# Optimization experiments

Measured on AMD Instinct MI355X. Metric: run time of the kernel, lower is better.

The kernel has to match this reference:

```python
import jax, jax.numpy as jnp
import numpy as np

B, DIM, H = 65536, 1024, 16
HD = DIM // H  # head dim = 64


def setup_inputs() -> dict:
    key = jax.random.key(0)
    ks = jax.random.split(key, 6)
    x = jax.random.normal(ks[0], (B, DIM), dtype=jnp.float32)
    y = jax.random.normal(ks[1], (B, DIM), dtype=jnp.float32)
    mask = jnp.zeros((B,), dtype=jnp.bool_)  # unused by the module
    # Parameters (qkv_bias=False -> no bias on q/kv; proj has bias)
    Wq = jax.random.normal(ks[2], (DIM, DIM), dtype=jnp.float32) * 0.02
    Wkv = jax.random.normal(ks[3], (DIM, 2 * DIM), dtype=jnp.float32) * 0.02
    Wproj = jax.random.normal(ks[4], (DIM, DIM), dtype=jnp.float32) * 0.02
    bproj = jax.random.normal(ks[5], (DIM,), dtype=jnp.float32) * 0.02
    return {"x": x, "y": y, "mask": mask, "Wq": Wq, "Wkv": Wkv,
            "Wproj": Wproj, "bproj": bproj}


def reference(x, y, mask, Wq, Wkv, Wproj, bproj):
    # mask is accepted but unused, matching the original module.
    scale = HD ** (-0.5)
    q = x @ Wq                      # [B, DIM]
    kv = y @ Wkv                    # [B, 2*DIM]
    k, v = jnp.split(kv, 2, axis=-1)
    # b (h d) -> b h d
    q = q.reshape(B, H, HD) * scale  # first scale (q *= scale)
    k = k.reshape(B, H, HD)
    v = v.reshape(B, H, HD)
    # per-head dot product, scaled AGAIN (faithful to original double-scale)
    dots = jnp.einsum("bhd,bhd->bh", q, k) * scale  # [B, H]
    attn = jax.nn.softmax(dots, axis=-1)             # softmax over heads
    out = attn[..., None] * v                        # [B, H, HD]
    out = out.reshape(B, DIM)                        # b h d -> b (h d)
    return out @ Wproj + bproj
```

## Files before the change

kernel.cpp:

```cpp
#include <hip/hip_runtime.h>

typedef unsigned short ushort_t;
typedef unsigned int   uint_t;

typedef ushort_t u16x8  __attribute__((ext_vector_type(8)));
typedef __bf16   bf16x8 __attribute__((ext_vector_type(8)));
typedef float    f32x4  __attribute__((ext_vector_type(4)));

#define DIMSZ 1024

__device__ __forceinline__ ushort_t f2bf(float f) {
  uint_t u = __builtin_bit_cast(uint_t, f);
  u += 0x7fffu + ((u >> 16) & 1u);
  return (ushort_t)(u >> 16);
}
__device__ __forceinline__ float bf2f(ushort_t h) {
  uint_t u = ((uint_t)h) << 16;
  return __builtin_bit_cast(float, u);
}
__device__ __forceinline__ void lds_load16(const void* g, void* l) {
  __builtin_amdgcn_global_load_lds((const __attribute__((address_space(1))) void*)g,
                                   (__attribute__((address_space(3))) void*)l, 16, 0, 0);
}
#define SCHED0() __builtin_amdgcn_sched_barrier(0)
#define WBAR() do { SCHED0(); __builtin_amdgcn_s_barrier(); SCHED0(); } while (0)

__global__ __launch_bounds__(256) void wtrans(const float* __restrict__ src, int ld,
                                              ushort_t* __restrict__ dst) {
  __shared__ ushort_t tile[32][33];
  const int bx = blockIdx.x, by = blockIdx.y;
  const int tx = threadIdx.x & 31, ty = threadIdx.x >> 5;
#pragma unroll
  for (int i = 0; i < 32; i += 8)
    tile[ty + i][tx] = f2bf(src[(size_t)(by * 32 + ty + i) * ld + bx * 32 + tx]);
  __syncthreads();
#pragma unroll
  for (int i = 0; i < 32; i += 8)
    dst[(size_t)(bx * 32 + ty + i) * 1024 + by * 32 + tx] = tile[tx][ty + i];
}

__global__ __launch_bounds__(256) void cvt_bf16(const float* __restrict__ s,
                                                ushort_t* __restrict__ d) {
  const size_t n8 = (size_t)65536 * 1024 / 8;
  const size_t stride = (size_t)gridDim.x * 256;
  for (size_t i = (size_t)blockIdx.x * 256 + threadIdx.x; i < n8; i += stride) {
    f32x4 f0 = *(const f32x4*)(s + i * 8);
    f32x4 f1 = *(const f32x4*)(s + i * 8 + 4);
    u16x8 o;
#pragma unroll
    for (int j = 0; j < 4; ++j) { o[j] = f2bf(f0[j]); o[4 + j] = f2bf(f1[j]); }
    *(u16x8*)(d + i * 8) = o;
  }
}

__global__ __launch_bounds__(256) void softmax16(float* __restrict__ d) {
  const int row = blockIdx.x * 256 + threadIdx.x;
  f32x4 v[4];
#pragma unroll
  for (int i = 0; i < 4; ++i) v[i] = *(const f32x4*)(d + (size_t)row * 16 + i * 4);
  float m = v[0][0];
#pragma unroll
  for (int i = 0; i < 4; ++i)
#pragma unroll
    for (int j = 0; j < 4; ++j) m = fmaxf(m, v[i][j]);
  float sum = 0.f;
#pragma unroll
  for (int i = 0; i < 4; ++i)
#pragma unroll
    for (int j = 0; j < 4; ++j) { v[i][j] = expf(v[i][j] - m); sum += v[i][j]; }
  const float r = 1.f / sum;
#pragma unroll
  for (int i = 0; i < 4; ++i) {
#pragma unroll
    for (int j = 0; j < 4; ++j) v[i][j] *= r;
    *(f32x4*)(d + (size_t)row * 16 + i * 4) = v[i];
  }
}

__global__ __launch_bounds__(256) void abk(const ushort_t* __restrict__ kvb,
                                           const float* __restrict__ at,
                                           ushort_t* __restrict__ ab) {
  const size_t stride = (size_t)gridDim.x * 256;
  for (size_t g = (size_t)blockIdx.x * 256 + threadIdx.x; g < (size_t)8388608; g += stride) {
    const int row = (int)(g >> 7), c8 = (int)(g & 127);
    const float sc = at[(size_t)row * 16 + (c8 >> 3)];
    u16x8 v8 = *(const u16x8*)(kvb + (size_t)row * 2048 + 1024 + c8 * 8);
    u16x8 o;
#pragma unroll
    for (int j = 0; j < 8; ++j) o[j] = f2bf(bf2f(v8[j]) * sc);
    *(u16x8*)(ab + (size_t)row * 1024 + c8 * 8) = o;
  }
}

template <int EPI>
__global__ __launch_bounds__(512, 2) void gemm8(const ushort_t* __restrict__ A,
                                                const ushort_t* __restrict__ Bt,
                                                void* __restrict__ Cv,
                                                const float* __restrict__ bias,
                                                const ushort_t* __restrict__ kvp,
                                                float* __restrict__ dots,
                                                int ldc, int ncol_lg2) {
  __shared__ ushort_t lds[65536];
  const int t = threadIdx.x;
  const int nb8 = gridDim.x >> 3;
  const int nbid = (blockIdx.x & 7) * nb8 + (blockIdx.x >> 3);
  const int n0 = (nbid & ((1 << ncol_lg2) - 1)) * 256;
  const int m0 = (nbid >> ncol_lg2) * 256;
  const int w = t >> 6, lane = t & 63;
  const int wm = w >> 2, wn = w & 3;
  const int lr = lane & 15, lk = lane >> 4;

  const int sr = lane >> 3;
  const int scsw = ((lane & 7) * 16) ^ ((sr & 7) << 4);
  const ushort_t* aS = A + (size_t)(m0 + w * 8 + sr) * DIMSZ + (scsw >> 1);
  const ushort_t* bS = Bt + (size_t)(n0 + w * 8 + sr) * DIMSZ + (scsw >> 1);

  const int cbe0 = ((lk * 16) ^ ((lr & 7) << 4)) >> 1;
  const int cbe1 = ((64 + lk * 16) ^ ((lr & 7) << 4)) >> 1;
  const int aRowB = (wm * 128 + lr) * 64;
  const int bRowB = 16384 + (wn * 64 + lr) * 64;

  f32x4 acc[8][4];
  const f32x4 zf = {0.f, 0.f, 0.f, 0.f};
#pragma unroll
  for (int i = 0; i < 8; ++i)
#pragma unroll
    for (int j = 0; j < 4; ++j) acc[i][j] = zf;
  bf16x8 a[4][2], b[4][2];

#define STG(cc, tt) do {                                                    \
    _Pragma("unroll") for (int i_ = 0; i_ < 4; ++i_)                        \
      lds_load16(aS + (size_t)i_ * 64 * DIMSZ + (tt) * 64,                  \
                 lds + (cc) * 32768 + (i_ * 64 + w * 8) * 64);              \
    _Pragma("unroll") for (int i_ = 0; i_ < 4; ++i_)                        \
      lds_load16(bS + (size_t)i_ * 64 * DIMSZ + (tt) * 64,                  \
                 lds + (cc) * 32768 + 16384 + (i_ * 64 + w * 8) * 64);      \
  } while (0)
#define LDA4(cc, mq) do {                                                   \
    const ushort_t* Lp = lds + (cc) * 32768 + aRowB + (mq) * 4096;          \
    _Pragma("unroll") for (int j = 0; j < 4; ++j) {                         \
      a[j][0] = *(const bf16x8*)(Lp + j * 1024 + cbe0);                     \
      a[j][1] = *(const bf16x8*)(Lp + j * 1024 + cbe1); } } while (0)
#define LDB4(cc) do {                                                       \
    const ushort_t* Lp = lds + (cc) * 32768 + bRowB;                        \
    _Pragma("unroll") for (int ni = 0; ni < 4; ++ni) {                      \
      b[ni][0] = *(const bf16x8*)(Lp + ni * 1024 + cbe0);                   \
      b[ni][1] = *(const bf16x8*)(Lp + ni * 1024 + cbe1); } } while (0)
#define MMQ(mb) do {                                                        \
    _Pragma("unroll") for (int j = 0; j < 4; ++j)                           \
    _Pragma("unroll") for (int ni = 0; ni < 4; ++ni)                        \
    _Pragma("unroll") for (int ks = 0; ks < 2; ++ks)                        \
      acc[(mb) + j][ni] = __builtin_amdgcn_mfma_f32_16x16x32_bf16(          \
          a[j][ks], b[ni][ks], acc[(mb) + j][ni], 0, 0, 0); } while (0)
#define TILE(S, VM, tv, cc) do {                                            \
    LDB4(cc);                                                               \
    LDA4(cc, 0);                                                            \
    __builtin_amdgcn_s_setprio(1); MMQ(0); __builtin_amdgcn_s_setprio(0);   \
    LDA4(cc, 1);                                                            \
    __builtin_amdgcn_s_setprio(1); MMQ(4); __builtin_amdgcn_s_setprio(0);   \
    WBAR();                                                                 \
    if (S) STG(cc, (tv) + 2);                                               \
    if ((VM) == 8)      asm volatile("s_waitcnt vmcnt(8)" ::: "memory");    \
    else if ((VM) == 0) asm volatile("s_waitcnt vmcnt(0)" ::: "memory");    \
    WBAR();                                                                 \
  } while (0)

  STG(0, 0); STG(1, 1);
  asm volatile("s_waitcnt vmcnt(8)" ::: "memory");
  WBAR();

  for (int tt = 0; tt < 7; ++tt) {
    const int t0 = tt * 2;
    TILE(1, 8, t0, 0);
    TILE(1, 8, t0 + 1, 1);
  }
  TILE(0, 0, 14, 0);
  TILE(0, -1, 15, 1);

#undef TILE
#undef MMQ
#undef LDB4
#undef LDA4
#undef STG

  if constexpr (EPI == 0) {
    ushort_t* Cp = (ushort_t*)Cv;
    ushort_t* ep = lds + w * 8192;
#pragma unroll
    for (int mq = 0; mq < 2; ++mq)
#pragma unroll
      for (int j = 0; j < 4; ++j)
#pragma unroll
        for (int ni = 0; ni < 4; ++ni)
#pragma unroll
          for (int r = 0; r < 4; ++r) {
            const int row = mq * 64 + j * 16 + lk * 4 + r;
            const int ce = ((ni * 16 + lr) * 2) ^ ((row & 7) << 4);
            ep[row * 64 + (ce >> 1)] = f2bf(acc[mq * 4 + j][ni][r]);
          }
#pragma unroll
    for (int rr = 0; rr < 16; ++rr) {
      const int row = rr * 8 + (lane >> 3);
      const int ce = ((lane & 7) * 16) ^ ((lane >> 3) << 4);
      u16x8 vv = *(const u16x8*)(ep + row * 64 + (ce >> 1));
      *(u16x8*)(Cp + (size_t)(m0 + wm * 128 + row) * ldc + n0 + wn * 64 + (lane & 7) * 8) = vv;
    }
  } else if constexpr (EPI == 1) {
    float* Op = (float*)Cv;
    float bb[4];
#pragma unroll
    for (int ni = 0; ni < 4; ++ni) bb[ni] = bias[n0 + wn * 64 + ni * 16 + lr];
#pragma unroll
    for (int mq = 0; mq < 2; ++mq)
#pragma unroll
      for (int j = 0; j < 4; ++j)
#pragma unroll
        for (int ni = 0; ni < 4; ++ni)
#pragma unroll
          for (int r = 0; r < 4; ++r)
            Op[(size_t)(m0 + wm * 128 + mq * 64 + j * 16 + lk * 4 + r) * 1024 +
               n0 + wn * 64 + ni * 16 + lr] = acc[mq * 4 + j][ni][r] + bb[ni];
  } else {
    const int h = (n0 >> 6) + wn;
    ushort_t* kw = lds + w * 8192;
    const int rsub = lane >> 3, c8 = (lane & 7) * 8;
    const ushort_t* kS = kvp + (size_t)(m0 + wm * 128 + rsub) * 2048 + h * 64 + c8;
#pragma unroll
    for (int i = 0; i < 16; ++i)
      lds_load16(kS + (size_t)i * 8 * 2048, kw + i * 512);
    asm volatile("s_waitcnt vmcnt(0)" ::: "memory");
#pragma unroll
    for (int mq = 0; mq < 2; ++mq)
#pragma unroll
      for (int j = 0; j < 4; ++j)
#pragma unroll
        for (int r = 0; r < 4; ++r) {
          const int row = mq * 64 + j * 16 + lk * 4 + r;
          float p = 0.f;
#pragma unroll
          for (int ni = 0; ni < 4; ++ni)
            p += acc[mq * 4 + j][ni][r] * bf2f(kw[row * 64 + ni * 16 + lr]);
#pragma unroll
          for (int off = 1; off < 16; off <<= 1) p += __shfl_xor(p, off, 16);
          if (lr == 0)
            dots[(size_t)(m0 + wm * 128 + row) * 16 + h] = p * 0.015625f;
        }
  }
}

extern "C" void kernel_launch(void* const* d_in, const int* in_sizes, int n_in,
                              void* d_out, int out_size, void* d_ws, size_t ws_size,
                              hipStream_t stream) {
  const float* x   = (const float*)d_in[0];
  const float* y   = (const float*)d_in[1];
  const float* Wq  = (const float*)d_in[3];
  const float* Wkv = (const float*)d_in[4];
  const float* Wp  = (const float*)d_in[5];
  const float* bp  = (const float*)d_in[6];
  (void)in_sizes; (void)n_in; (void)out_size; (void)ws_size;

  char* ws = (char*)d_ws;
  ushort_t* Wqt   = (ushort_t*)(ws);
  ushort_t* Wkvt  = (ushort_t*)(ws + (2ull   << 20));
  ushort_t* Wpt   = (ushort_t*)(ws + (6ull   << 20));
  float*    dotsb = (float*)   (ws + (8ull   << 20));
  ushort_t* kvb   = (ushort_t*)(ws + (12ull  << 20));
  ushort_t* actb  = (ushort_t*)(ws + (268ull << 20));

  wtrans<<<dim3(32, 32), 256, 0, stream>>>(Wq, 1024, Wqt);
  wtrans<<<dim3(64, 32), 256, 0, stream>>>(Wkv, 2048, Wkvt);
  wtrans<<<dim3(32, 32), 256, 0, stream>>>(Wp, 1024, Wpt);

  cvt_bf16<<<4096, 256, 0, stream>>>(y, actb);
  gemm8<0><<<2048, 512, 0, stream>>>(actb, Wkvt, kvb, nullptr, nullptr, nullptr, 2048, 3);

  cvt_bf16<<<4096, 256, 0, stream>>>(x, actb);
  gemm8<2><<<1024, 512, 0, stream>>>(actb, Wqt, nullptr, nullptr, kvb, dotsb, 1024, 2);

  softmax16<<<256, 256, 0, stream>>>(dotsb);

  abk<<<2048, 256, 0, stream>>>(kvb, dotsb, actb);

  gemm8<1><<<1024, 512, 0, stream>>>(actb, Wpt, d_out, bp, nullptr, nullptr, 1024, 2);
}
```

Measured before the change: 882.2 us.

## Shrink GEMM tile to 256x128 with K=32 triple-buffered LDS pipeline

The GEMM kernel moves from a 256x256 output tile with K-step 64 and double buffering to a 256x128 tile with K-step 32 and three LDS buffers. This cuts shared memory from 128KB to about 72KB per block so more blocks fit per CU (launch bounds raised to 4), and the grid is doubled. Each wave now computes 64x64 instead of 128x64, which lowers register pressure but also lowers arithmetic intensity and increases redundant global loads of A. The epilogues are adjusted for the new per-wave tile.

```diff
diff --git a/kernel.cpp b/kernel.cpp
--- a/kernel.cpp
+++ b/kernel.cpp
@@ -93,117 +93,112 @@
 }
 
 template <int EPI>
-__global__ __launch_bounds__(512, 2) void gemm8(const ushort_t* __restrict__ A,
+__global__ __launch_bounds__(512, 4) void gemm8(const ushort_t* __restrict__ A,
                                                 const ushort_t* __restrict__ Bt,
                                                 void* __restrict__ Cv,
                                                 const float* __restrict__ bias,
                                                 const ushort_t* __restrict__ kvp,
                                                 float* __restrict__ dots,
                                                 int ldc, int ncol_lg2) {
-  __shared__ ushort_t lds[65536];
+  __shared__ ushort_t lds[36864];
   const int t = threadIdx.x;
   const int nb8 = gridDim.x >> 3;
   const int nbid = (blockIdx.x & 7) * nb8 + (blockIdx.x >> 3);
-  const int n0 = (nbid & ((1 << ncol_lg2) - 1)) * 256;
+  const int n0 = (nbid & ((1 << ncol_lg2) - 1)) * 128;
   const int m0 = (nbid >> ncol_lg2) * 256;
   const int w = t >> 6, lane = t & 63;
-  const int wm = w >> 2, wn = w & 3;
+  const int wm = w >> 1, wn = w & 1;
   const int lr = lane & 15, lk = lane >> 4;
-
-  const int sr = lane >> 3;
-  const int scsw = ((lane & 7) * 16) ^ ((sr & 7) << 4);
-  const ushort_t* aS = A + (size_t)(m0 + w * 8 + sr) * DIMSZ + (scsw >> 1);
-  const ushort_t* bS = Bt + (size_t)(n0 + w * 8 + sr) * DIMSZ + (scsw >> 1);
-
-  const int cbe0 = ((lk * 16) ^ ((lr & 7) << 4)) >> 1;
-  const int cbe1 = ((64 + lk * 16) ^ ((lr & 7) << 4)) >> 1;
-  const int aRowB = (wm * 128 + lr) * 64;
-  const int bRowB = 16384 + (wn * 64 + lr) * 64;
-
-  f32x4 acc[8][4];
+  const int w512 = w * 512;
+
+  const int srw = lane >> 2;
+  const int scsw = (((lane & 3) * 16) ^ ((srw & 3) << 4)) >> 1;
+  const ushort_t* aS = A + (size_t)(m0 + w * 16 + srw) * DIMSZ + scsw;
+  const ushort_t* bS = Bt + (size_t)(n0 + w * 16 + srw) * DIMSZ + scsw;
+
+  const int cbe = ((lk * 16) ^ ((lr & 3) << 4)) >> 1;
+  const int aRow = (wm * 64 + lr) * 32;
+  const int bRow = 8192 + (wn * 64 + lr) * 32;
+
+  f32x4 acc[4][4];
   const f32x4 zf = {0.f, 0.f, 0.f, 0.f};
 #pragma unroll
-  for (int i = 0; i < 8; ++i)
+  for (int i = 0; i < 4; ++i)
 #pragma unroll
     for (int j = 0; j < 4; ++j) acc[i][j] = zf;
-  bf16x8 a[4][2], b[4][2];
-
-#define STG(cc, tt) do {                                                    \
-    _Pragma("unroll") for (int i_ = 0; i_ < 4; ++i_)                        \
-      lds_load16(aS + (size_t)i_ * 64 * DIMSZ + (tt) * 64,                  \
-                 lds + (cc) * 32768 + (i_ * 64 + w * 8) * 64);              \
-    _Pragma("unroll") for (int i_ = 0; i_ < 4; ++i_)                        \
-      lds_load16(bS + (size_t)i_ * 64 * DIMSZ + (tt) * 64,                  \
-                 lds + (cc) * 32768 + 16384 + (i_ * 64 + w * 8) * 64);      \
-  } while (0)
-#define LDA4(cc, mq) do {                                                   \
-    const ushort_t* Lp = lds + (cc) * 32768 + aRowB + (mq) * 4096;          \
-    _Pragma("unroll") for (int j = 0; j < 4; ++j) {                         \
-      a[j][0] = *(const bf16x8*)(Lp + j * 1024 + cbe0);                     \
-      a[j][1] = *(const bf16x8*)(Lp + j * 1024 + cbe1); } } while (0)
-#define LDB4(cc) do {                                                       \
-    const ushort_t* Lp = lds + (cc) * 32768 + bRowB;                        \
-    _Pragma("unroll") for (int ni = 0; ni < 4; ++ni) {                      \
-      b[ni][0] = *(const bf16x8*)(Lp + ni * 1024 + cbe0);                   \
-      b[ni][1] = *(const bf16x8*)(Lp + ni * 1024 + cbe1); } } while (0)
-#define MMQ(mb) do {                                                        \
+  bf16x8 a[4], b[2];
+
+#define STG_A(bb, tt) do {                                                  \
+    lds_load16(aS + (tt) * 32, lds + (bb) * 12288 + w512);                  \
+    lds_load16(aS + 131072 + (tt) * 32, lds + (bb) * 12288 + 4096 + w512);  \
+  } while (0)
+#define STG_B(bb, tt)                                                       \
+    lds_load16(bS + (tt) * 32, lds + (bb) * 12288 + 8192 + w512)
+#define LDA4(bb) do {                                                       \
     _Pragma("unroll") for (int j = 0; j < 4; ++j)                           \
-    _Pragma("unroll") for (int ni = 0; ni < 4; ++ni)                        \
-    _Pragma("unroll") for (int ks = 0; ks < 2; ++ks)                        \
-      acc[(mb) + j][ni] = __builtin_amdgcn_mfma_f32_16x16x32_bf16(          \
-          a[j][ks], b[ni][ks], acc[(mb) + j][ni], 0, 0, 0); } while (0)
-#define TILE(S, VM, tv, cc) do {                                            \
-    LDB4(cc);                                                               \
-    LDA4(cc, 0);                                                            \
+      a[j] = *(const bf16x8*)(lds + (bb) * 12288 + aRow + j * 512 + cbe);   \
+  } while (0)
+#define LDB2(bb, nb) do {                                                   \
+    _Pragma("unroll") for (int ni = 0; ni < 2; ++ni)                        \
+      b[ni] = *(const bf16x8*)(lds + (bb) * 12288 + bRow + ((nb) + ni) * 512 + cbe); \
+  } while (0)
+#define MMQ(nb) do {                                                        \
+    _Pragma("unroll") for (int j = 0; j < 4; ++j)                           \
+    _Pragma("unroll") for (int ni = 0; ni < 2; ++ni)                        \
+      acc[j][(nb) + ni] = __builtin_amdgcn_mfma_f32_16x16x32_bf16(          \
+          a[j], b[ni], acc[j][(nb) + ni], 0, 0, 0); } while (0)
+#define TILE(S, tv, c, n2) do {                                             \
+    LDA4(c); LDB2(c, 0);                                                    \
+    if (S) STG_A(n2, (tv) + 2);                                             \
+    WBAR();                                                                 \
     __builtin_amdgcn_s_setprio(1); MMQ(0); __builtin_amdgcn_s_setprio(0);   \
-    LDA4(cc, 1);                                                            \
-    __builtin_amdgcn_s_setprio(1); MMQ(4); __builtin_amdgcn_s_setprio(0);   \
-    WBAR();                                                                 \
-    if (S) STG(cc, (tv) + 2);                                               \
-    if ((VM) == 8)      asm volatile("s_waitcnt vmcnt(8)" ::: "memory");    \
-    else if ((VM) == 0) asm volatile("s_waitcnt vmcnt(0)" ::: "memory");    \
-    WBAR();                                                                 \
-  } while (0)
-
-  STG(0, 0); STG(1, 1);
-  asm volatile("s_waitcnt vmcnt(8)" ::: "memory");
+    WBAR();                                                                 \
+    LDB2(c, 2);                                                             \
+    if (S) STG_B(n2, (tv) + 2);                                             \
+    WBAR();                                                                 \
+    __builtin_amdgcn_s_setprio(1); MMQ(2); __builtin_amdgcn_s_setprio(0);   \
+    if (S) { asm volatile("s_waitcnt vmcnt(3)" ::: "memory"); }             \
+    else if ((tv) == 30) { asm volatile("s_waitcnt vmcnt(0)" ::: "memory"); } \
+    WBAR();                                                                 \
+  } while (0)
+
+  STG_A(0, 0); STG_B(0, 0);
+  STG_A(1, 1); STG_B(1, 1);
+  asm volatile("s_waitcnt vmcnt(3)" ::: "memory");
   WBAR();
 
-  for (int tt = 0; tt < 7; ++tt) {
-    const int t0 = tt * 2;
-    TILE(1, 8, t0, 0);
-    TILE(1, 8, t0 + 1, 1);
-  }
-  TILE(0, 0, 14, 0);
-  TILE(0, -1, 15, 1);
+#pragma unroll
+  for (int tt = 0; tt < 30; ++tt) TILE(1, tt, tt % 3, (tt + 2) % 3);
+  TILE(0, 30, 0, 0);
+  TILE(0, 31, 1, 0);
 
 #undef TILE
 #undef MMQ
-#undef LDB4
+#undef LDB2
 #undef LDA4
-#undef STG
+#undef STG_B
+#undef STG_A
 
   if constexpr (EPI == 0) {
     ushort_t* Cp = (ushort_t*)Cv;
-    ushort_t* ep = lds + w * 8192;
-#pragma unroll
-    for (int mq = 0; mq < 2; ++mq)
-#pragma unroll
-      for (int j = 0; j < 4; ++j)
-#pragma unroll
-        for (int ni = 0; ni < 4; ++ni)
-#pragma unroll
-          for (int r = 0; r < 4; ++r) {
-            const int row = mq * 64 + j * 16 + lk * 4 + r;
-            const int ce = ((ni * 16 + lr) * 2) ^ ((row & 7) << 4);
-            ep[row * 64 + (ce >> 1)] = f2bf(acc[mq * 4 + j][ni][r]);
-          }
-#pragma unroll
-    for (int rr = 0; rr < 16; ++rr) {
+    ushort_t* ep = lds + w * 4096;
+#pragma unroll
+    for (int j = 0; j < 4; ++j)
+#pragma unroll
+      for (int ni = 0; ni < 4; ++ni)
+#pragma unroll
+        for (int r = 0; r < 4; ++r) {
+          const int row = j * 16 + lk * 4 + r;
+          const int ce = ((ni * 16 + lr) * 2) ^ ((row & 7) << 4);
+          ep[row * 64 + (ce >> 1)] = f2bf(acc[j][ni][r]);
+        }
+    __builtin_amdgcn_s_barrier();
+#pragma unroll
+    for (int rr = 0; rr < 8; ++rr) {
       const int row = rr * 8 + (lane >> 3);
       const int ce = ((lane & 7) * 16) ^ ((lane >> 3) << 4);
       u16x8 vv = *(const u16x8*)(ep + row * 64 + (ce >> 1));
-      *(u16x8*)(Cp + (size_t)(m0 + wm * 128 + row) * ldc + n0 + wn * 64 + (lane & 7) * 8) = vv;
+      *(u16x8*)(Cp + (size_t)(m0 + wm * 64 + row) * ldc + n0 + wn * 64 + (lane & 7) * 8) = vv;
     }
   } else if constexpr (EPI == 1) {
     float* Op = (float*)Cv;
@@ -211,40 +206,36 @@
 #pragma unroll
     for (int ni = 0; ni < 4; ++ni) bb[ni] = bias[n0 + wn * 64 + ni * 16 + lr];
 #pragma unroll
-    for (int mq = 0; mq < 2; ++mq)
-#pragma unroll
-      for (int j = 0; j < 4; ++j)
-#pragma unroll
-        for (int ni = 0; ni < 4; ++ni)
-#pragma unroll
-          for (int r = 0; r < 4; ++r)
-            Op[(size_t)(m0 + wm * 128 + mq * 64 + j * 16 + lk * 4 + r) * 1024 +
-               n0 + wn * 64 + ni * 16 + lr] = acc[mq * 4 + j][ni][r] + bb[ni];
+    for (int j = 0; j < 4; ++j)
+#pragma unroll
+      for (int ni = 0; ni < 4; ++ni)
+#pragma unroll
+        for (int r = 0; r < 4; ++r)
+          Op[(size_t)(m0 + wm * 64 + j * 16 + lk * 4 + r) * 1024 +
+             n0 + wn * 64 + ni * 16 + lr] = acc[j][ni][r] + bb[ni];
   } else {
     const int h = (n0 >> 6) + wn;
-    ushort_t* kw = lds + w * 8192;
+    ushort_t* kw = lds + w * 4096;
     const int rsub = lane >> 3, c8 = (lane & 7) * 8;
-    const ushort_t* kS = kvp + (size_t)(m0 + wm * 128 + rsub) * 2048 + h * 64 + c8;
-#pragma unroll
-    for (int i = 0; i < 16; ++i)
+    const ushort_t* kS = kvp + (size_t)(m0 + wm * 64 + rsub) * 2048 + h * 64 + c8;
+#pragma unroll
+    for (int i = 0; i < 8; ++i)
       lds_load16(kS + (size_t)i * 8 * 2048, kw + i * 512);
     asm volatile("s_waitcnt vmcnt(0)" ::: "memory");
 #pragma unroll
-    for (int mq = 0; mq < 2; ++mq)
-#pragma unroll
-      for (int j = 0; j < 4; ++j)
-#pragma unroll
-        for (int r = 0; r < 4; ++r) {
-          const int row = mq * 64 + j * 16 + lk * 4 + r;
-          float p = 0.f;
-#pragma unroll
-          for (int ni = 0; ni < 4; ++ni)
-            p += acc[mq * 4 + j][ni][r] * bf2f(kw[row * 64 + ni * 16 + lr]);
-#pragma unroll
-          for (int off = 1; off < 16; off <<= 1) p += __shfl_xor(p, off, 16);
-          if (lr == 0)
-            dots[(size_t)(m0 + wm * 128 + row) * 16 + h] = p * 0.015625f;
-        }
+    for (int j = 0; j < 4; ++j)
+#pragma unroll
+      for (int r = 0; r < 4; ++r) {
+        const int row = j * 16 + lk * 4 + r;
+        float p = 0.f;
+#pragma unroll
+        for (int ni = 0; ni < 4; ++ni)
+          p += acc[j][ni][r] * bf2f(kw[row * 64 + ni * 16 + lr]);
+#pragma unroll
+        for (int off = 1; off < 16; off <<= 1) p += __shfl_xor(p, off, 16);
+        if (lr == 0)
+          dots[(size_t)(m0 + wm * 64 + row) * 16 + h] = p * 0.015625f;
+      }
   }
 }
 
@@ -272,14 +263,14 @@
   wtrans<<<dim3(32, 32), 256, 0, stream>>>(Wp, 1024, Wpt);
 
   cvt_bf16<<<4096, 256, 0, stream>>>(y, actb);
-  gemm8<0><<<2048, 512, 0, stream>>>(actb, Wkvt, kvb, nullptr, nullptr, nullptr, 2048, 3);
+  gemm8<0><<<4096, 512, 0, stream>>>(actb, Wkvt, kvb, nullptr, nullptr, nullptr, 2048, 4);
 
   cvt_bf16<<<4096, 256, 0, stream>>>(x, actb);
-  gemm8<2><<<1024, 512, 0, stream>>>(actb, Wqt, nullptr, nullptr, kvb, dotsb, 1024, 2);
+  gemm8<2><<<2048, 512, 0, stream>>>(actb, Wqt, nullptr, nullptr, kvb, dotsb, 1024, 3);
 
   softmax16<<<256, 256, 0, stream>>>(dotsb);
 
   abk<<<2048, 256, 0, stream>>>(kvb, dotsb, actb);
 
-  gemm8<1><<<1024, 512, 0, stream>>>(actb, Wpt, d_out, bp, nullptr, nullptr, 1024, 2);
-}
+  gemm8<1><<<2048, 512, 0, stream>>>(actb, Wpt, d_out, bp, nullptr, nullptr, 1024, 3);
+}
```

Result: faster. 864.3 us (-2.0%).
